# Kernel optimization log

Measured on AMD Instinct MI355X. Metric: run time of the kernel, lower is better.

## Reference

```python
import jax, jax.numpy as jnp
import numpy as np

B, S, E, H, L, V = 64, 512, 256, 256, 5, 50001  # vocab_size+1 rows, padding_idx=0
GC = 256  # gcn_hidden
NC = [10, 5]


def lstm_dir(x, Wih, Whh, b):
    # x: [B,S,D]; Wih: [4H,D]; Whh: [4H,H]; b: [4H] (= b_ih + b_hh)
    h0 = jnp.zeros((x.shape[0], Whh.shape[1]), x.dtype)
    def step(carry, xt):
        h, c = carry
        g = xt @ Wih.T + h @ Whh.T + b
        i, f, gg, o = jnp.split(g, 4, axis=-1)  # torch gate order i,f,g,o
        c = jax.nn.sigmoid(f) * c + jax.nn.sigmoid(i) * jnp.tanh(gg)
        h = jax.nn.sigmoid(o) * jnp.tanh(c)
        return (h, c), h
    _, hs = jax.lax.scan(step, (h0, h0), jnp.swapaxes(x, 0, 1))
    return jnp.swapaxes(hs, 0, 1)  # [B,S,H]


def layer_norm(x, g, b, eps=1e-5):
    mu = jnp.mean(x, -1, keepdims=True)
    var = jnp.mean((x - mu) ** 2, -1, keepdims=True)
    return (x - mu) * jax.lax.rsqrt(var + eps) * g + b


def banded_adj_matmul(x, mask):
    # adj has only super/sub-diagonal ones, masked by m_i*m_j, row-normalized (+1e-8).
    m = mask
    m_next = jnp.pad(m[:, 1:], ((0, 0), (0, 1)))
    m_prev = jnp.pad(m[:, :-1], ((0, 0), (1, 0)))
    rs = m * (m_prev + m_next) + 1e-8  # row sums
    c_next = (m * m_next / rs)[:, :, None]
    c_prev = (m * m_prev / rs)[:, :, None]
    x_next = jnp.pad(x[:, 1:], ((0, 0), (0, 1), (0, 0)))
    x_prev = jnp.pad(x[:, :-1], ((0, 0), (1, 0), (0, 0)))
    return c_next * x_next + c_prev * x_prev


def gcn_layer(x, mask, W, b, gamma, beta):
    h = banded_adj_matmul(x, mask)
    h = h @ W.T + b
    h = h + x  # in_dim == out_dim -> residual
    return jax.nn.relu(layer_norm(h, gamma, beta))


def setup_inputs() -> dict:
    key = jax.random.key(0)
    ks = jax.random.split(key, 24)
    rn = lambda k, sh, s=0.05: jax.random.normal(k, sh, jnp.float32) * s
    seq = jax.random.randint(ks[0], (B, S), 0, V, jnp.int32)
    mask = jnp.ones((B, S), jnp.float32)
    aux = rn(ks[1], (B, 6), 1.0)
    emb_table = rn(ks[2], (V, E), 0.1).at[0].set(0.0)  # padding_idx=0
    Wih0 = rn(ks[3], (2, 4 * H, E))
    Whh0 = rn(ks[4], (2, 4 * H, H))
    b0 = rn(ks[5], (2, 4 * H))
    Wih = rn(ks[6], (L - 1, 2, 4 * H, 2 * H))
    Whh = rn(ks[7], (L - 1, 2, 4 * H, H))
    bL = rn(ks[8], (L - 1, 2, 4 * H))
    gcn_W = rn(ks[9], (3, GC, E))
    gcn_b = rn(ks[10], (3, GC))
    gcn_gamma = jnp.ones((3, GC), jnp.float32)
    gcn_beta = jnp.zeros((3, GC), jnp.float32)
    fusion = 2 * H + GC + 6
    fc1_W = rn(ks[11], (512, fusion))
    fc1_b = rn(ks[12], (512,))
    fc2_W = rn(ks[13], (256, 512))
    fc2_b = rn(ks[14], (256,))
    head0_W = rn(ks[15], (NC[0], 256))
    head0_b = rn(ks[16], (NC[0],))
    head1_W = rn(ks[17], (NC[1], 256))
    head1_b = rn(ks[18], (NC[1],))
    return dict(seq=seq, mask=mask, aux=aux, emb_table=emb_table, Wih0=Wih0,
                Whh0=Whh0, b0=b0, Wih=Wih, Whh=Whh, bL=bL, gcn_W=gcn_W,
                gcn_b=gcn_b, gcn_gamma=gcn_gamma, gcn_beta=gcn_beta,
                fc1_W=fc1_W, fc1_b=fc1_b, fc2_W=fc2_W, fc2_b=fc2_b,
                head0_W=head0_W, head0_b=head0_b, head1_W=head1_W, head1_b=head1_b)


def reference(seq, mask, aux, emb_table, Wih0, Whh0, b0, Wih, Whh, bL,
              gcn_W, gcn_b, gcn_gamma, gcn_beta, fc1_W, fc1_b, fc2_W, fc2_b,
              head0_W, head0_b, head1_W, head1_b):
    emb = emb_table[seq]  # [B,S,E]; dropout = identity (eval)
    # 5-layer bidirectional LSTM
    out = emb
    for l in range(L):
        wih, whh, b = (Wih0, Whh0, b0) if l == 0 else (Wih[l - 1], Whh[l - 1], bL[l - 1])
        fwd = lstm_dir(out, wih[0], whh[0], b[0])
        bwd = jnp.flip(lstm_dir(jnp.flip(out, 1), wih[1], whh[1], b[1]), 1)
        out = jnp.concatenate([fwd, bwd], -1)  # [B,S,2H]
    lstm_out = out * mask[:, :, None]
    denom = jnp.clip(jnp.sum(mask, 1, keepdims=True), 1e-8)
    lstm_feat = jnp.sum(lstm_out, 1) / denom  # [B,2H]
    # GCN stack over banded adjacency
    g = emb
    for i in range(3):
        g = gcn_layer(g, mask, gcn_W[i], gcn_b[i], gcn_gamma[i], gcn_beta[i])
    g = g * mask[:, :, None]
    gcn_feat = jnp.sum(g, 1) / denom  # [B,GC]
    fused = jnp.concatenate([lstm_feat, gcn_feat, aux], 1)
    s = jax.nn.relu(fused @ fc1_W.T + fc1_b)
    s = jax.nn.relu(s @ fc2_W.T + fc2_b)
    return (s @ head0_W.T + head0_b, s @ head1_W.T + head1_b)
```

## Files before the change

### kernel.cpp

```cpp
#include <hip/hip_runtime.h>
#include <stdint.h>
#include <stddef.h>

typedef __bf16 bf16;
typedef __bf16 bf16x8 __attribute__((ext_vector_type(8)));
typedef __bf16 bf16x4 __attribute__((ext_vector_type(4)));
typedef float  f32x4  __attribute__((ext_vector_type(4)));
typedef int    v4i    __attribute__((ext_vector_type(4)));

#define NB   64
#define NS   512
#define NE   256
#define NH   256
#define NL   5
#define NGC  256
#define FUSION 774

__device__ __forceinline__ float sigm(float x) {
    return __fdividef(1.f, 1.f + __expf(-x));
}
__device__ __forceinline__ float tanh_(float x) {
    return __fdividef(2.f, 1.f + __expf(-2.f * x)) - 1.f;
}

__device__ __forceinline__ void gload_lds16(const void* g, void* l) {
    __builtin_amdgcn_global_load_lds(
        (const __attribute__((address_space(1))) void*)g,
        (__attribute__((address_space(3))) void*)l,
        16, 0, 0);
}

__global__ void k_cvt(const float* __restrict__ src, bf16* __restrict__ dst, int n4) {
    int i = blockIdx.x * 256 + threadIdx.x;
    if (i >= n4) return;
    f32x4 v = ((const f32x4*)src)[i];
    bf16x4 o;
    o[0] = (bf16)v[0]; o[1] = (bf16)v[1]; o[2] = (bf16)v[2]; o[3] = (bf16)v[3];
    ((bf16x4*)dst)[i] = o;
}

__global__ void k_embed(const int* __restrict__ seq, const float* __restrict__ table,
                        float* __restrict__ ef, bf16* __restrict__ eb) {
    int t  = blockIdx.x * 256 + threadIdx.x;
    int bs = t >> 6;
    int c4 = (t & 63) << 2;
    int row = seq[bs];
    f32x4 v = *(const f32x4*)(table + (size_t)row * NE + c4);
    *(f32x4*)(ef + (size_t)bs * NE + c4) = v;
    bf16x4 o;
    o[0] = (bf16)v[0]; o[1] = (bf16)v[1]; o[2] = (bf16)v[2]; o[3] = (bf16)v[3];
    *(bf16x4*)(eb + (size_t)bs * NE + c4) = o;
}

__global__ __launch_bounds__(256, 2)
void k_gemm(const bf16* __restrict__ A, const bf16* __restrict__ W,
            const float* __restrict__ bias, void* __restrict__ Cout,
            int M, int N, int K, int out_mode) {
    __shared__ __align__(16) bf16 sA[128 * 64];
    __shared__ __align__(16) bf16 sB[128 * 64];
    const int mblk = M >> 7;
    int bm = blockIdx.x % mblk;
    int bn = blockIdx.x / mblk;
    int m0 = bm << 7, n0 = bn << 7;
    int tid  = threadIdx.x;
    int wave = tid >> 6, lane = tid & 63;
    int wm = wave >> 1, wn = wave & 1;
    int l15 = lane & 15, quad = lane >> 4;

    f32x4 acc[4][4] = {};

    const int r0 = tid >> 3;
    const int c0 = (tid & 7) * 8;
    const bf16* Ab = A + (size_t)(m0 + r0) * K + c0;
    const bf16* Wb = W + (size_t)(n0 + r0) * K + c0;
    bf16* sAd = sA + tid * 8;
    bf16* sBd = sB + tid * 8;

    for (int k0 = 0; k0 < K; k0 += 64) {
#pragma unroll
        for (int i = 0; i < 4; i++) {
            gload_lds16(Ab + (size_t)(i * 32) * K + k0, sAd + i * 2048);
            gload_lds16(Wb + (size_t)(i * 32) * K + k0, sBd + i * 2048);
        }
        __syncthreads();
#pragma unroll
        for (int kk = 0; kk < 2; kk++) {
            bf16x8 af[4], bfr[4];
#pragma unroll
            for (int mt = 0; mt < 4; mt++)
                af[mt] = *(const bf16x8*)(sA + (wm * 64 + mt * 16 + l15) * 64 + kk * 32 + quad * 8);
#pragma unroll
            for (int nt = 0; nt < 4; nt++)
                bfr[nt] = *(const bf16x8*)(sB + (wn * 64 + nt * 16 + l15) * 64 + kk * 32 + quad * 8);
#pragma unroll
            for (int mt = 0; mt < 4; mt++)
#pragma unroll
                for (int nt = 0; nt < 4; nt++)
                    acc[mt][nt] = __builtin_amdgcn_mfma_f32_16x16x32_bf16(af[mt], bfr[nt], acc[mt][nt], 0, 0, 0);
        }
        __syncthreads();
    }
#pragma unroll
    for (int mt = 0; mt < 4; mt++) {
#pragma unroll
        for (int nt = 0; nt < 4; nt++) {
            int col = n0 + wn * 64 + nt * 16 + l15;
            float bv = bias[col];
            int row0 = m0 + wm * 64 + mt * 16 + quad * 4;
#pragma unroll
            for (int r4 = 0; r4 < 4; r4++) {
                float v = acc[mt][nt][r4] + bv;
                int r = row0 + r4;
                if (out_mode == 3) {
                    int tt = r & (NS - 1), b = r >> 9;
                    int dd = col >> 10, g = (col >> 8) & 3, j = col & 255;
                    ((bf16*)Cout)[(((((size_t)tt * 64 + b) * 2 + dd) * 256 + j) << 2) + g] = (bf16)v;
                } else {
                    ((float*)Cout)[(size_t)r * N + col] = v;
                }
            }
        }
    }
}

__global__ void k_prep_i8(const float* __restrict__ Whh0, const float* __restrict__ WhhL,
                          signed char* __restrict__ Wp8, float* __restrict__ scales) {
    int gw = blockIdx.x * 4 + (threadIdx.x >> 6);
    int lane = threadIdx.x & 63;
    int row = gw & 1023;
    int d = (gw >> 10) & 1;
    int layer = gw >> 11;
    const float* src = (layer == 0)
        ? (Whh0 + ((size_t)d * 1024 + row) * 256)
        : (WhhL + (((size_t)(layer - 1) * 2 + d) * 1024 + row) * 256);
    f32x4 v = *(const f32x4*)(src + lane * 4);
    float am = fmaxf(fmaxf(fabsf(v[0]), fabsf(v[1])), fmaxf(fabsf(v[2]), fabsf(v[3])));
#pragma unroll
    for (int off = 32; off >= 1; off >>= 1) am = fmaxf(am, __shfl_xor(am, off));
    am = fmaxf(am, 1e-8f);
    float inv = 127.f / am;
    int q0 = (int)__builtin_rintf(v[0] * inv);
    int q1 = (int)__builtin_rintf(v[1] * inv);
    int q2 = (int)__builtin_rintf(v[2] * inv);
    int q3 = (int)__builtin_rintf(v[3] * inv);
    uint32_t packed = (q0 & 255) | ((q1 & 255) << 8) | ((q2 & 255) << 16) | ((q3 & 255) << 24);
    int g = row >> 8, rem = row & 255;
    int w = rem >> 4, l15r = rem & 15;
    int k = lane * 4;
    int kt = k >> 6, q = (k >> 4) & 3, j = k & 15;
    size_t cell = ((size_t)layer * 2 + d) * 256 + (w * 4 + g) * 4 + kt;
    *(uint32_t*)(Wp8 + cell * 1024 + (q * 16 + l15r) * 16 + j) = packed;
    if (lane == 0)
        scales[((size_t)layer * 2 + d) * 1024 + row] = am * (1.f / (127.f * 127.f));
}

__global__ __launch_bounds__(512, 2)
void k_lstm_i8(const bf16* __restrict__ G,
               const signed char* __restrict__ Wp8,
               const float* __restrict__ sc,
               bf16* __restrict__ io_out)
{
    __shared__ signed char hs[2][2 * 4 * 80];

    const int d   = blockIdx.x & 1;
    const int bg  = blockIdx.x >> 1;
    const int tid = threadIdx.x;
    const int w = tid >> 6, lane = tid & 63;
    const int l15 = lane & 15, quad = lane >> 4;
    const int b_loc = quad & 1;
    const int jg    = quad >> 1;
    const int b = bg * 2 + b_loc;
    const int j = (w + jg * 8) * 16 + l15;

    v4i Wr[2][4][4];
#pragma unroll
    for (int sl = 0; sl < 2; sl++) {
        const int ws = w + sl * 8;
        const signed char* wb = Wp8 + ((size_t)d * 256 + ws * 16) * 1024 + lane * 16;
#pragma unroll
        for (int g = 0; g < 4; g++)
#pragma unroll
            for (int kt = 0; kt < 4; kt++)
                Wr[sl][g][kt] = *(const v4i*)(wb + (g * 4 + kt) * 1024);
    }
#pragma unroll
    for (int sl = 0; sl < 2; sl++)
#pragma unroll
        for (int g = 0; g < 4; g++)
#pragma unroll
            for (int kt = 0; kt < 4; kt++)
                asm volatile("" : "+v"(Wr[sl][g][kt]));

    float scv[4];
#pragma unroll
    for (int g = 0; g < 4; g++)
        scv[g] = sc[d * 1024 + g * 256 + j];

    const int goffs = ((b * 2 + d) * 256 + j) * 4;
    const size_t iob = (size_t)b * NS * 512 + d * 256 + j;

    const int hwr = (b_loc * 4 + (j >> 6)) * 80 + (j & 63);
    const int hrd = (((l15 >> 2) & 1) * 4 + (l15 & 3)) * 80 + quad * 16;
    const int rr = l15 & 3;

    float cst = 0.f;

    bf16x4 gq0 = *(const bf16x4*)(G + (size_t)(d ? (NS - 1) : 0) * 131072 + goffs);
    bf16x4 gq1 = *(const bf16x4*)(G + (size_t)(d ? (NS - 2) : 1) * 131072 + goffs);

    for (int t = 0; t < NS; t++) {
        const int rb = (t + 1) & 1, wbuf = t & 1;

        bf16x4 gq2 = gq0;
        if (t + 2 < NS) {
            const size_t t2 = (size_t)(d ? (NS - 3 - t) : (t + 2)) * 131072;
            gq2 = *(const bf16x4*)(G + t2 + goffs);
        }

        v4i acc[2][4] = {};
        if (t > 0) {
            v4i chunk = *(const v4i*)&hs[rb][hrd];
            v4i a[4];
#pragma unroll
            for (int kt = 0; kt < 4; kt++) {
                a[kt][0] = (rr == kt) ? chunk[0] : 0;
                a[kt][1] = (rr == kt) ? chunk[1] : 0;
                a[kt][2] = (rr == kt) ? chunk[2] : 0;
                a[kt][3] = (rr == kt) ? chunk[3] : 0;
            }
#pragma unroll
            for (int sl = 0; sl < 2; sl++)
#pragma unroll
                for (int g = 0; g < 4; g++)
#pragma unroll
                    for (int kt = 0; kt < 4; kt++)
                        acc[sl][g] = __builtin_amdgcn_mfma_i32_16x16x64_i8(a[kt], Wr[sl][g][kt], acc[sl][g], 0, 0, 0);
        }

        int s[4];
#pragma unroll
        for (int g = 0; g < 4; g++) {
            int s0 = acc[0][g][0] + acc[0][g][1] + acc[0][g][2] + acc[0][g][3];
            int s1 = acc[1][g][0] + acc[1][g][1] + acc[1][g][2] + acc[1][g][3];
            s[g] = jg ? s1 : s0;
        }
        float pi = (float)s[0] * scv[0] + (float)gq0[0];
        float pf = (float)s[1] * scv[1] + (float)gq0[1];
        float pg = (float)s[2] * scv[2] + (float)gq0[2];
        float po = (float)s[3] * scv[3] + (float)gq0[3];
        float ig = sigm(pi), fg = sigm(pf), gc = tanh_(pg), og = sigm(po);
        float c = fg * cst + ig * gc;
        cst = c;
        float hh = og * tanh_(c);
        const int tcur = d ? (NS - 1 - t) : t;
        io_out[iob + (size_t)tcur * 512] = (bf16)hh;
        hs[wbuf][hwr] = (signed char)(int)__builtin_rintf(hh * 127.f);

        gq0 = gq1; gq1 = gq2;

        asm volatile("s_waitcnt lgkmcnt(0)" ::: "memory");
        __builtin_amdgcn_s_barrier();
        asm volatile("" ::: "memory");
    }
}

__global__ void k_banded(const float* __restrict__ x, const float* __restrict__ mask,
                         bf16* __restrict__ outb) {
    int t  = blockIdx.x * 256 + threadIdx.x;
    int bs = t >> 6;
    int c4 = (t & 63) << 2;
    int s = bs & (NS - 1);
    float m  = mask[bs];
    float mn = (s < NS - 1) ? mask[bs + 1] : 0.f;
    float mp = (s > 0)      ? mask[bs - 1] : 0.f;
    float rs = m * (mp + mn) + 1e-8f;
    float cn = m * mn / rs;
    float cp = m * mp / rs;
    f32x4 vn = {}, vp = {};
    if (s < NS - 1) vn = *(const f32x4*)(x + (size_t)(bs + 1) * NGC + c4);
    if (s > 0)      vp = *(const f32x4*)(x + (size_t)(bs - 1) * NGC + c4);
    bf16x4 o;
#pragma unroll
    for (int i = 0; i < 4; i++) o[i] = (bf16)(cn * vn[i] + cp * vp[i]);
    *(bf16x4*)(outb + (size_t)bs * NGC + c4) = o;
}

__global__ void k_gcnpost(const float* __restrict__ gemm_out, const float* __restrict__ x,
                          const float* __restrict__ gamma, const float* __restrict__ beta,
                          float* __restrict__ outx) {
    int row  = blockIdx.x * 4 + (threadIdx.x >> 6);
    int lane = threadIdx.x & 63;
    const float* h  = gemm_out + (size_t)row * NGC;
    const float* xr = x + (size_t)row * NGC;
    f32x4 hv = *(const f32x4*)(h + lane * 4);
    f32x4 xv = *(const f32x4*)(xr + lane * 4);
    f32x4 v;
#pragma unroll
    for (int i = 0; i < 4; i++) v[i] = hv[i] + xv[i];
    float sum = v[0] + v[1] + v[2] + v[3];
#pragma unroll
    for (int off = 32; off >= 1; off >>= 1) sum += __shfl_xor(sum, off);
    float mu = sum * (1.f / NGC);
    float sq = 0.f;
    f32x4 dv;
#pragma unroll
    for (int i = 0; i < 4; i++) { dv[i] = v[i] - mu; sq += dv[i] * dv[i]; }
#pragma unroll
    for (int off = 32; off >= 1; off >>= 1) sq += __shfl_xor(sq, off);
    float inv = rsqrtf(sq * (1.f / NGC) + 1e-5f);
    f32x4 o;
#pragma unroll
    for (int i = 0; i < 4; i++) {
        int c = lane * 4 + i;
        float y = dv[i] * inv * gamma[c] + beta[c];
        o[i] = fmaxf(y, 0.f);
    }
    *(f32x4*)(outx + (size_t)row * NGC + lane * 4) = o;
}

__global__ void k_pool_bf16(const bf16* __restrict__ src, const float* __restrict__ mask,
                            float* __restrict__ feat) {
    int b = blockIdx.x, f = threadIdx.x;
    float acc = 0.f, dm = 0.f;
    for (int t = 0; t < NS; t++) {
        float m = mask[b * NS + t];
        acc += m * (float)src[((size_t)b * NS + t) * 512 + f];
        dm += m;
    }
    feat[b * 512 + f] = acc / fmaxf(dm, 1e-8f);
}
__global__ void k_pool_f32(const float* __restrict__ src, const float* __restrict__ mask,
                           float* __restrict__ feat) {
    int b = blockIdx.x, f = threadIdx.x;
    float acc = 0.f, dm = 0.f;
    for (int t = 0; t < NS; t++) {
        float m = mask[b * NS + t];
        acc += m * src[((size_t)b * NS + t) * NGC + f];
        dm += m;
    }
    feat[b * NGC + f] = acc / fmaxf(dm, 1e-8f);
}

__global__ __launch_bounds__(512)
void k_head(const float* __restrict__ lfeat, const float* __restrict__ gfeat,
            const float* __restrict__ aux,
            const float* __restrict__ fc1W, const float* __restrict__ fc1b,
            const float* __restrict__ fc2W, const float* __restrict__ fc2b,
            const float* __restrict__ h0W, const float* __restrict__ h0b,
            const float* __restrict__ h1W, const float* __restrict__ h1b,
            float* __restrict__ out) {
    __shared__ float fused[FUSION];
    __shared__ float s1[512];
    __shared__ float s2[256];
    int m = blockIdx.x, tid = threadIdx.x;
    if (tid < 512) fused[tid] = lfeat[m * 512 + tid];
    if (tid < 256) fused[512 + tid] = gfeat[m * 256 + tid];
    if (tid < 6)   fused[768 + tid] = aux[m * 6 + tid];
    __syncthreads();
    {
        float a = fc1b[tid];
        const float* w = fc1W + (size_t)tid * FUSION;
        for (int k = 0; k < FUSION; k++) a += w[k] * fused[k];
        s1[tid] = fmaxf(a, 0.f);
    }
    __syncthreads();
    if (tid < 256) {
        float a = fc2b[tid];
        const float* w = fc2W + (size_t)tid * 512;
        for (int k = 0; k < 512; k++) a += w[k] * s1[k];
        s2[tid] = fmaxf(a, 0.f);
    }
    __syncthreads();
    if (tid < 15) {
        if (tid < 10) {
            float a = h0b[tid];
            const float* w = h0W + (size_t)tid * 256;
            for (int k = 0; k < 256; k++) a += w[k] * s2[k];
            out[m * 10 + tid] = a;
        } else {
            int n = tid - 10;
            float a = h1b[n];
            const float* w = h1W + (size_t)n * 256;
            for (int k = 0; k < 256; k++) a += w[k] * s2[k];
            out[640 + m * 5 + n] = a;
        }
    }
}

extern "C" void kernel_launch(void* const* d_in, const int* in_sizes, int n_in,
                              void* d_out, int out_size, void* d_ws, size_t ws_size,
                              hipStream_t stream) {
    const int*   seq   = (const int*)d_in[0];
    const float* mask  = (const float*)d_in[1];
    const float* aux   = (const float*)d_in[2];
    const float* table = (const float*)d_in[3];
    const float* Wih0  = (const float*)d_in[4];
    const float* Whh0  = (const float*)d_in[5];
    const float* b0    = (const float*)d_in[6];
    const float* WihL  = (const float*)d_in[7];
    const float* WhhL  = (const float*)d_in[8];
    const float* bL    = (const float*)d_in[9];
    const float* gcnW  = (const float*)d_in[10];
    const float* gcnb  = (const float*)d_in[11];
    const float* gcnG  = (const float*)d_in[12];
    const float* gcnBe = (const float*)d_in[13];
    const float* fc1W  = (const float*)d_in[14];
    const float* fc1b  = (const float*)d_in[15];
    const float* fc2W  = (const float*)d_in[16];
    const float* fc2b  = (const float*)d_in[17];
    const float* h0W   = (const float*)d_in[18];
    const float* h0b   = (const float*)d_in[19];
    const float* h1W   = (const float*)d_in[20];
    const float* h1b   = (const float*)d_in[21];
    float* outp = (float*)d_out;

    char* ws = (char*)d_ws;
    const size_t MROWS = (size_t)NB * NS;
    signed char* Wp8 = (signed char*)(ws + 0);
    float* wsc     = (float*)(ws + 2621440);
    bf16*  Wbf     = (bf16*) (ws + 2662400);
    bf16*  wb0     = Wbf;
    bf16*  wbL     = Wbf + 524288;
    bf16*  wgcn    = Wbf + 524288 + 4194304;
    bf16*  emb_b   = (bf16*) (ws + 33554432);
    bf16*  io0     = (bf16*) (ws + 50331648);
    bf16*  io1     = (bf16*) (ws + 83886080);
    char*  Greg    =          ws + 117440512;
    bf16*  G       = (bf16*)  Greg;
    float* lfeat   = (float*)(ws + 251658240);
    float* gfeat   = (float*)(ws + 251789312);
    float* gcnA  = (float*)(Greg + 0);
    float* gcnB_ = (float*)(Greg + 33554432);
    float* ggemm = (float*)(Greg + 67108864);
    bf16*  gtmp  = (bf16*) (Greg + 100663296);
    (void)ws_size; (void)n_in; (void)in_sizes; (void)out_size;

    k_cvt<<<dim3(512),  dim3(256), 0, stream>>>(Wih0, wb0, 131072);
    k_cvt<<<dim3(4096), dim3(256), 0, stream>>>(WihL, wbL, 1048576);
    k_cvt<<<dim3(192),  dim3(256), 0, stream>>>(gcnW, wgcn, 49152);
    k_prep_i8<<<dim3(2560), dim3(256), 0, stream>>>(Whh0, WhhL, Wp8, wsc);

    k_embed<<<dim3(8192), dim3(256), 0, stream>>>(seq, table, gcnA, emb_b);

    const float* xcur = gcnA;
    float* xnxt[3] = {gcnB_, gcnA, gcnB_};
    for (int i = 0; i < 3; i++) {
        k_banded<<<dim3(8192), dim3(256), 0, stream>>>(xcur, mask, gtmp);
        k_gemm<<<dim3((MROWS / 128) * (NGC / 128)), dim3(256), 0, stream>>>(
            gtmp, wgcn + (size_t)i * NGC * NGC, gcnb + i * NGC, ggemm,
            (int)MROWS, NGC, NGC, 0);
        k_gcnpost<<<dim3(8192), dim3(256), 0, stream>>>(
            ggemm, xcur, gcnG + i * NGC, gcnBe + i * NGC, xnxt[i]);
        xcur = xnxt[i];
    }
    k_pool_f32<<<dim3(NB), dim3(NGC), 0, stream>>>(xcur, mask, gfeat);

    const bf16* Xin = emb_b;
    int Kin = NE;
    bf16* ios[2] = {io0, io1};
    for (int l = 0; l < NL; l++) {
        const bf16* wih = l ? (wbL + (size_t)(l - 1) * 1048576) : wb0;
        const float* bias = l ? (bL + (size_t)(l - 1) * 2048) : b0;
        k_gemm<<<dim3((MROWS / 128) * (2048 / 128)), dim3(256), 0, stream>>>(
            Xin, wih, bias, G, (int)MROWS, 2048, Kin, 3);
        bf16* lio = ios[l & 1];
        k_lstm_i8<<<dim3(64), dim3(512), 0, stream>>>(
            G, Wp8 + (size_t)l * 524288, wsc + (size_t)l * 2048, lio);
        Xin = lio;
        Kin = 512;
    }
    k_pool_bf16<<<dim3(NB), dim3(512), 0, stream>>>(ios[(NL - 1) & 1], mask, lfeat);

    k_head<<<dim3(NB), dim3(512), 0, stream>>>(
        lfeat, gfeat, aux, fc1W, fc1b, fc2W, fc2b, h0W, h0b, h1W, h1b, outp);
}
```

Baseline: 3.514 ms.

## Store gate preactivations row-major and peel first LSTM timestep

The input-projection GEMM now writes gate preactivations in plain row-major [B*S, 2048] bf16 instead of a time-major, gate-interleaved scattered layout. This makes the GEMM epilogue stores coalesced. In exchange, the LSTM kernel now does four strided scalar loads per step instead of one 8-byte vector load. The first timestep is peeled out so the MFMA recurrent path runs without the t>0 branch.

```diff
diff --git a/kernel.cpp b/kernel.cpp
--- a/kernel.cpp
+++ b/kernel.cpp
@@ -111,10 +111,8 @@
             for (int r4 = 0; r4 < 4; r4++) {
                 float v = acc[mt][nt][r4] + bv;
                 int r = row0 + r4;
-                if (out_mode == 3) {
-                    int tt = r & (NS - 1), b = r >> 9;
-                    int dd = col >> 10, g = (col >> 8) & 3, j = col & 255;
-                    ((bf16*)Cout)[(((((size_t)tt * 64 + b) * 2 + dd) * 256 + j) << 2) + g] = (bf16)v;
+                if (out_mode == 1) {
+                    ((bf16*)Cout)[(size_t)r * N + col] = (bf16)v;
                 } else {
                     ((float*)Cout)[(size_t)r * N + col] = v;
                 }
@@ -154,6 +152,11 @@
         scales[((size_t)layer * 2 + d) * 1024 + row] = am * (1.f / (127.f * 127.f));
 }
 
+struct G4 { bf16 g0, g1, g2, g3; };
+__device__ __forceinline__ G4 loadG4(const bf16* p) {
+    G4 r; r.g0 = p[0]; r.g1 = p[256]; r.g2 = p[512]; r.g3 = p[768]; return r;
+}
+
 __global__ __launch_bounds__(512, 2)
 void k_lstm_i8(const bf16* __restrict__ G,
                const signed char* __restrict__ Wp8,
@@ -196,7 +199,7 @@
     for (int g = 0; g < 4; g++)
         scv[g] = sc[d * 1024 + g * 256 + j];
 
-    const int goffs = ((b * 2 + d) * 256 + j) * 4;
+    const bf16* gbase = G + d * 1024 + j;
     const size_t iob = (size_t)b * NS * 512 + d * 256 + j;
 
     const int hwr = (b_loc * 4 + (j >> 6)) * 80 + (j & 63);
@@ -205,20 +208,38 @@
 
     float cst = 0.f;
 
-    bf16x4 gq0 = *(const bf16x4*)(G + (size_t)(d ? (NS - 1) : 0) * 131072 + goffs);
-    bf16x4 gq1 = *(const bf16x4*)(G + (size_t)(d ? (NS - 2) : 1) * 131072 + goffs);
-
-    for (int t = 0; t < NS; t++) {
+    G4 gcur = loadG4(gbase + (size_t)(b * 512 + (d ? (NS - 1) : 0)) * 2048);
+    G4 gnxt = loadG4(gbase + (size_t)(b * 512 + (d ? (NS - 2) : 1)) * 2048);
+
+    {
+        G4 gfut = loadG4(gbase + (size_t)(b * 512 + (d ? (NS - 3) : 2)) * 2048);
+        float pi = (float)gcur.g0, pf = (float)gcur.g1;
+        float pg = (float)gcur.g2, po = (float)gcur.g3;
+        float ig = sigm(pi), gc = tanh_(pg), og = sigm(po);
+        (void)pf;
+        float c = ig * gc;
+        cst = c;
+        float hh = og * tanh_(c);
+        const int tcur = d ? (NS - 1) : 0;
+        io_out[iob + (size_t)tcur * 512] = (bf16)hh;
+        hs[0][hwr] = (signed char)(int)__builtin_rintf(hh * 127.f);
+        gcur = gnxt; gnxt = gfut;
+        asm volatile("s_waitcnt lgkmcnt(0)" ::: "memory");
+        __builtin_amdgcn_s_barrier();
+        asm volatile("" ::: "memory");
+    }
+
+    for (int t = 1; t < NS; t++) {
         const int rb = (t + 1) & 1, wbuf = t & 1;
 
-        bf16x4 gq2 = gq0;
+        G4 gfut = gcur;
         if (t + 2 < NS) {
-            const size_t t2 = (size_t)(d ? (NS - 3 - t) : (t + 2)) * 131072;
-            gq2 = *(const bf16x4*)(G + t2 + goffs);
+            const int tt2 = d ? (NS - 3 - t) : (t + 2);
+            gfut = loadG4(gbase + (size_t)(b * 512 + tt2) * 2048);
         }
 
         v4i acc[2][4] = {};
-        if (t > 0) {
+        {
             v4i chunk = *(const v4i*)&hs[rb][hrd];
             v4i a[4];
 #pragma unroll
@@ -244,10 +265,10 @@
             int s1 = acc[1][g][0] + acc[1][g][1] + acc[1][g][2] + acc[1][g][3];
             s[g] = jg ? s1 : s0;
         }
-        float pi = (float)s[0] * scv[0] + (float)gq0[0];
-        float pf = (float)s[1] * scv[1] + (float)gq0[1];
-        float pg = (float)s[2] * scv[2] + (float)gq0[2];
-        float po = (float)s[3] * scv[3] + (float)gq0[3];
+        float pi = (float)s[0] * scv[0] + (float)gcur.g0;
+        float pf = (float)s[1] * scv[1] + (float)gcur.g1;
+        float pg = (float)s[2] * scv[2] + (float)gcur.g2;
+        float po = (float)s[3] * scv[3] + (float)gcur.g3;
         float ig = sigm(pi), fg = sigm(pf), gc = tanh_(pg), og = sigm(po);
         float c = fg * cst + ig * gc;
         cst = c;
@@ -256,7 +277,7 @@
         io_out[iob + (size_t)tcur * 512] = (bf16)hh;
         hs[wbuf][hwr] = (signed char)(int)__builtin_rintf(hh * 127.f);
 
-        gq0 = gq1; gq1 = gq2;
+        gcur = gnxt; gnxt = gfut;
 
         asm volatile("s_waitcnt lgkmcnt(0)" ::: "memory");
         __builtin_amdgcn_s_barrier();
@@ -462,7 +483,7 @@
         const bf16* wih = l ? (wbL + (size_t)(l - 1) * 1048576) : wb0;
         const float* bias = l ? (bL + (size_t)(l - 1) * 2048) : b0;
         k_gemm<<<dim3((MROWS / 128) * (2048 / 128)), dim3(256), 0, stream>>>(
-            Xin, wih, bias, G, (int)MROWS, 2048, Kin, 3);
+            Xin, wih, bias, G, (int)MROWS, 2048, Kin, 1);
         bf16* lio = ios[l & 1];
         k_lstm_i8<<<dim3(64), dim3(512), 0, stream>>>(
             G, Wp8 + (size_t)l * 524288, wsc + (size_t)l * 2048, lio);
```

New measurement: 3.781 ms. 1.08x slower.
